# Kernel optimization log

Hardware: AMD Instinct MI355X
Metric: run time of the kernel (lower is better)

## Reference

```python
import math
import jax, jax.numpy as jnp
import numpy as np

B, N, D = 32, 1025, 768
K, CD, TD = 64, 128, 256  # num_clusters, cluster_dim, token_dim
REG = 0.1
NUM_ITERS = 5


def setup_inputs() -> dict:
    key = jax.random.key(0)
    ks = jax.random.split(key, 8)
    x = jax.random.normal(ks[0], (B, N, D), dtype=jnp.float32)
    # Linear params (torch nn.Linear: y = x @ W.T + b; we store W already transposed as [in, out])
    Wf = jax.random.normal(ks[1], (D, CD), dtype=jnp.float32) / math.sqrt(D)
    bf = jnp.zeros((CD,), dtype=jnp.float32)
    Ws = jax.random.normal(ks[2], (D, K), dtype=jnp.float32) / math.sqrt(D)
    bs = jnp.zeros((K,), dtype=jnp.float32)
    Wt = jax.random.normal(ks[3], (D, TD), dtype=jnp.float32) / math.sqrt(D)
    bt = jnp.zeros((TD,), dtype=jnp.float32)
    anchors = jax.random.normal(ks[4], (K, CD), dtype=jnp.float32) * 0.1
    dust_bin = jnp.float32(1.0)
    sharpness = jnp.float32(5.0)
    return {"x": x, "Wf": Wf, "bf": bf, "Ws": Ws, "bs": bs, "Wt": Wt, "bt": bt,
            "anchors": anchors, "dust_bin": dust_bin, "sharpness": sharpness}


def _log_otp_solver(log_a, log_b, M, num_iters, reg):
    M = M / reg
    u = jnp.zeros_like(log_a)  # [B, K+1]
    v = jnp.zeros_like(log_b)  # [B, N-1]
    for _ in range(num_iters):
        u = log_a - jax.nn.logsumexp(M + v[:, None, :], axis=2)
        v = log_b - jax.nn.logsumexp(M + u[:, :, None], axis=1)
    return M + u[:, :, None] + v[:, None, :]


def reference(x, Wf, bf, Ws, bs, Wt, bt, anchors, dust_bin, sharpness):
    b, n, d = x.shape
    t_global = x[:, 0]            # [B, D]
    fi = x[:, 1:]                 # [B, N-1, D]
    f = fi @ Wf + bf              # [B, N-1, CD]
    s = jnp.swapaxes(fi @ Ws + bs, 1, 2)  # [B, K, N-1]
    t = t_global @ Wt + bt        # [B, TD]
    s = s * sharpness
    dust = jnp.broadcast_to(dust_bin, (b, 1, n - 1))
    s_aug = jnp.concatenate([s, dust], axis=1)  # [B, K+1, N-1]
    log_a = jnp.full((b, K + 1), -math.log(K + 1), dtype=x.dtype)
    log_b = jnp.full((b, n - 1), -math.log(n - 1), dtype=x.dtype)
    log_P = _log_otp_solver(log_a, log_b, s_aug, NUM_ITERS, REG)
    p = jnp.exp(log_P)[:, :-1, :]  # [B, K, N-1]
    # v_agg = sum_n p[b,k,n] * (2*f[b,n,:] - anchors[k,:])  (algebraic rewrite of the broadcast sum)
    v_agg = 2.0 * jnp.einsum('bkn,bnc->bkc', p, f) - p.sum(axis=2)[:, :, None] * anchors[None]
    v_local = v_agg.reshape(b, -1)            # [B, K*CD]
    f_out = jnp.concatenate([t, v_local], axis=-1)
    norm = jnp.maximum(jnp.linalg.norm(f_out, axis=-1, keepdims=True), 1e-12)
    return f_out / norm
```

## Files before the change

kernel.cpp:

```cpp
#include <hip/hip_runtime.h>
#include <math.h>


#define BATCH 32
#define NTOK  1025
#define DIM   768
#define KDIM  64
#define CDIM  128
#define TDIM  256
#define NM1   1024
#define ROWLEN 8448
#define NITER 5
#define INV_REG 10.0f
#define NS_AGG 8
#define LOG_A (-4.17438727f)
#define LOG_B (-6.93147181f)

typedef __attribute__((ext_vector_type(8))) short short8;
typedef __attribute__((ext_vector_type(4))) float floatx4;

typedef __attribute__((address_space(3))) unsigned int lds_uint;
typedef const __attribute__((address_space(1))) unsigned int glb_uint;

__device__ __forceinline__ void gload_lds16(const void* g, void* l) {
    __builtin_amdgcn_global_load_lds((glb_uint*)g, (lds_uint*)l, 16, 0, 0);
}

__device__ __forceinline__ unsigned short bf16_rne(float f) {
    unsigned u = __builtin_bit_cast(unsigned, f);
    unsigned r = u + 0x7FFFu + ((u >> 16) & 1u);
    return (unsigned short)(r >> 16);
}

__device__ __forceinline__ short8 cvt8(float4 a, float4 b) {
    short8 r;
    r[0] = (short)bf16_rne(a.x); r[1] = (short)bf16_rne(a.y);
    r[2] = (short)bf16_rne(a.z); r[3] = (short)bf16_rne(a.w);
    r[4] = (short)bf16_rne(b.x); r[5] = (short)bf16_rne(b.y);
    r[6] = (short)bf16_rne(b.z); r[7] = (short)bf16_rne(b.w);
    return r;
}

__global__ __launch_bounds__(256) void prep(
    const float* __restrict__ Wf, const float* __restrict__ Ws,
    const float* __restrict__ bf, const float* __restrict__ bs,
    const float* __restrict__ x, const float* __restrict__ Wt,
    short* __restrict__ W_pack, float* __restrict__ bias_all,
    float* __restrict__ tpart)
{
    __shared__ float xr[256];
    const int blk = blockIdx.x, tid = threadIdx.x;
    if (blk < 576) {
        int idx = blk * 256 + tid;
        int g    = idx / 6144;
        int rem  = idx - g * 6144;
        int nf   = rem >> 9;
        int rem2 = rem & 511;
        int lane = rem2 >> 3;
        int j    = rem2 & 7;
        int k = g * 32 + (lane >> 4) * 8 + j;
        int c = nf * 16 + (lane & 15);
        float v = (c < CDIM) ? Wf[(size_t)k * CDIM + c] : Ws[(size_t)k * KDIM + (c - CDIM)];
        W_pack[idx] = (short)bf16_rne(v);
        if (idx < 192) bias_all[idx] = (idx < CDIM) ? bf[idx] : bs[idx - CDIM];
    } else {
        int i = blk - 576;
        int b = i / 3, dy = i - b * 3;
        xr[tid] = x[(size_t)b * NTOK * DIM + (size_t)dy * 256 + tid];
        __syncthreads();
        float acc = 0.f;
        const float* wp = Wt + (size_t)dy * 256 * TDIM + tid;
#pragma unroll 8
        for (int d = 0; d < 256; ++d) acc = fmaf(xr[d], wp[(size_t)d * TDIM], acc);
        tpart[((size_t)dy * BATCH + b) * TDIM + tid] = acc;
    }
}

__global__ __launch_bounds__(256, 2) void gemm_fs(
    const float* __restrict__ x, const short* __restrict__ W_pack,
    const float* __restrict__ bias_all, const float* __restrict__ sharp_p,
    unsigned short* __restrict__ fT, float* __restrict__ Mmat)
{
    __shared__ __align__(16) short Bs[12288];
    __shared__ __align__(16) short As[4096];
    const int tid  = threadIdx.x;
    const int wave = tid >> 6, lane = tid & 63;
    const int quad = lane >> 4, lrow = lane & 15;
    const int R = blockIdx.x * 64 + wave * 16;

    const int arow = blockIdx.x * 64 + (tid >> 2);
    const float* asrc = x + ((size_t)(arow >> 10) * NTOK + 1 + (arow & 1023)) * DIM + (tid & 3) * 16;
    const int r    = (tid >> 2) & 15;
    const int seg  = tid & 3;
    const int kk_w = seg >> 1;
    const int q0   = (seg & 1) * 2;
    short* adst0 = &As[(((tid >> 6) * 2 + kk_w) * 64 + q0 * 16 + r) * 8];
    short* adst1 = &As[(((tid >> 6) * 2 + kk_w) * 64 + (q0 + 1) * 16 + r) * 8];

    floatx4 acc[12];
#pragma unroll
    for (int nf = 0; nf < 12; ++nf) acc[nf] = (floatx4){0.f, 0.f, 0.f, 0.f};

    float4 g0 = *(const float4*)(asrc);
    float4 g1 = *(const float4*)(asrc + 4);
    float4 g2 = *(const float4*)(asrc + 8);
    float4 g3 = *(const float4*)(asrc + 12);

    for (int ko = 0; ko < 12; ++ko) {
        __syncthreads();
        const short* bsrc = W_pack + ko * 12288 + tid * 8;
#pragma unroll
        for (int i = 0; i < 6; ++i)
            gload_lds16(bsrc + i * 2048, &Bs[i * 2048 + tid * 8]);
        *(short8*)adst0 = cvt8(g0, g1);
        *(short8*)adst1 = cvt8(g2, g3);
        if (ko < 11) {
            const float* ap = asrc + (ko + 1) * 64;
            g0 = *(const float4*)(ap);
            g1 = *(const float4*)(ap + 4);
            g2 = *(const float4*)(ap + 8);
            g3 = *(const float4*)(ap + 12);
        }
        __syncthreads();
#pragma unroll
        for (int kk = 0; kk < 2; ++kk) {
            short8 af = *(const short8*)&As[((wave * 2 + kk) * 64 + lane) * 8];
#pragma unroll
            for (int nf = 0; nf < 12; ++nf) {
                short8 bf8 = *(const short8*)&Bs[((kk * 12 + nf) * 64 + lane) * 8];
                acc[nf] = __builtin_amdgcn_mfma_f32_16x16x32_bf16(af, bf8, acc[nf], 0, 0, 0);
            }
        }
    }

    const float sc = sharp_p[0] * INV_REG;
    const int bb = R >> 10;
    const int tok = (R & 1023) + quad * 4;
#pragma unroll
    for (int nf = 0; nf < 12; ++nf) {
        const int c = nf * 16 + lrow;
        const float bias = bias_all[c];
        if (nf < 8) {
            ushort4 w;
            w.x = bf16_rne(acc[nf][0] + bias);
            w.y = bf16_rne(acc[nf][1] + bias);
            w.z = bf16_rne(acc[nf][2] + bias);
            w.w = bf16_rne(acc[nf][3] + bias);
            *(ushort4*)(fT + ((size_t)bb * CDIM + c) * NM1 + tok) = w;
        } else {
            const int k = c - CDIM;
            float4 w = make_float4((acc[nf][0] + bias) * sc, (acc[nf][1] + bias) * sc,
                                   (acc[nf][2] + bias) * sc, (acc[nf][3] + bias) * sc);
            *(float4*)(Mmat + ((size_t)bb * KDIM + k) * NM1 + tok) = w;
        }
    }
}

template<bool FIRST>
__global__ __launch_bounds__(256) void sink_u(
    const float* __restrict__ Mmat, const float* __restrict__ v_in,
    const float* __restrict__ dust_p, float* __restrict__ u_out)
{
    const int wv   = (blockIdx.x << 2) + (threadIdx.x >> 6);
    const int lane = threadIdx.x & 63;
    const int b = wv / 65, k = wv - b * 65;
    const float dustM = dust_p[0] * INV_REG;

    const float4* vp = (const float4*)(v_in + (size_t)b * NM1);
    float xs[16];
    if (k < 64) {
        const float4* Mp = (const float4*)(Mmat + ((size_t)b * KDIM + k) * NM1);
#pragma unroll
        for (int i = 0; i < 4; ++i) {
            float4 mv = Mp[i * 64 + lane];
            float4 vv = FIRST ? make_float4(0.f, 0.f, 0.f, 0.f) : vp[i * 64 + lane];
            xs[i * 4 + 0] = mv.x + vv.x;
            xs[i * 4 + 1] = mv.y + vv.y;
            xs[i * 4 + 2] = mv.z + vv.z;
            xs[i * 4 + 3] = mv.w + vv.w;
        }
    } else {
#pragma unroll
        for (int i = 0; i < 4; ++i) {
            float4 vv = FIRST ? make_float4(0.f, 0.f, 0.f, 0.f) : vp[i * 64 + lane];
            xs[i * 4 + 0] = dustM + vv.x;
            xs[i * 4 + 1] = dustM + vv.y;
            xs[i * 4 + 2] = dustM + vv.z;
            xs[i * 4 + 3] = dustM + vv.w;
        }
    }
    float m = xs[0];
#pragma unroll
    for (int i = 1; i < 16; ++i) m = fmaxf(m, xs[i]);
#pragma unroll
    for (int off = 1; off < 64; off <<= 1) m = fmaxf(m, __shfl_xor(m, off));
    float S = 0.f;
#pragma unroll
    for (int i = 0; i < 16; ++i) S += __expf(xs[i] - m);
#pragma unroll
    for (int off = 1; off < 64; off <<= 1) S += __shfl_xor(S, off);
    if (lane == 0) u_out[wv] = LOG_A - (m + __logf(S));
}

__global__ __launch_bounds__(128) void sink_v(
    const float* __restrict__ Mmat, const float* __restrict__ u_in,
    const float* __restrict__ dust_p, float* __restrict__ v_out)
{
    __shared__ float us[65];
    const int b = blockIdx.x, tid = threadIdx.x;
    const int n = blockIdx.y * 128 + tid;
    if (tid < 65) us[tid] = u_in[b * 65 + tid];
    __syncthreads();
    const float* Mb = Mmat + (size_t)b * KDIM * NM1 + n;
    float xs[64];
#pragma unroll
    for (int k = 0; k < 64; ++k) xs[k] = Mb[(size_t)k * NM1] + us[k];
    const float xd = dust_p[0] * INV_REG + us[64];
    float m = xd;
#pragma unroll
    for (int k = 0; k < 64; ++k) m = fmaxf(m, xs[k]);
    float S = __expf(xd - m);
#pragma unroll
    for (int k = 0; k < 64; ++k) S += __expf(xs[k] - m);
    v_out[(size_t)b * NM1 + n] = LOG_B - (m + __logf(S));
}

__global__ __launch_bounds__(256) void aggregate(
    const float* __restrict__ Mmat, const unsigned short* __restrict__ fT,
    const float* __restrict__ u_in, const float* __restrict__ v_in,
    float* __restrict__ vpart, float* __restrict__ rspart)
{
    __shared__ float us[KDIM];
    __shared__ float vsh[128];
    const int b = blockIdx.x, ns = blockIdx.y;
    const int tid = threadIdx.x;
    const int wave = tid >> 6, lane = tid & 63;
    const int quad = lane >> 4, lrow = lane & 15;

    if (tid < 64) us[tid] = u_in[b * 65 + tid];
    else if (tid < 192) vsh[tid - 64] = v_in[(size_t)b * NM1 + ns * 128 + (tid - 64)];
    __syncthreads();

    const int krow = wave * 16 + lrow;
    const float uk = us[krow];
    const float* Mrow = Mmat + ((size_t)b * KDIM + krow) * NM1 + ns * 128 + quad * 8;
    const unsigned short* fbase = fT + ((size_t)b * CDIM + lrow) * NM1 + ns * 128 + quad * 8;

    floatx4 acc[8];
#pragma unroll
    for (int nf = 0; nf < 8; ++nf) acc[nf] = (floatx4){0.f, 0.f, 0.f, 0.f};
    float rs = 0.f;

#pragma unroll
    for (int step = 0; step < 4; ++step) {
        const float* mp = Mrow + step * 32;
        float4 m0 = *(const float4*)(mp);
        float4 m1 = *(const float4*)(mp + 4);
        const int tb = step * 32 + quad * 8;
        float p[8];
        p[0] = __expf(m0.x + uk + vsh[tb + 0]);
        p[1] = __expf(m0.y + uk + vsh[tb + 1]);
        p[2] = __expf(m0.z + uk + vsh[tb + 2]);
        p[3] = __expf(m0.w + uk + vsh[tb + 3]);
        p[4] = __expf(m1.x + uk + vsh[tb + 4]);
        p[5] = __expf(m1.y + uk + vsh[tb + 5]);
        p[6] = __expf(m1.z + uk + vsh[tb + 6]);
        p[7] = __expf(m1.w + uk + vsh[tb + 7]);
        short8 afrag;
#pragma unroll
        for (int j = 0; j < 8; ++j) {
            rs += p[j];
            afrag[j] = (short)bf16_rne(p[j]);
        }
#pragma unroll
        for (int nf = 0; nf < 8; ++nf) {
            short8 bfrag = *(const short8*)(fbase + (size_t)nf * 16 * NM1 + step * 32);
            acc[nf] = __builtin_amdgcn_mfma_f32_16x16x32_bf16(afrag, bfrag, acc[nf], 0, 0, 0);
        }
    }

    rs += __shfl_xor(rs, 16);
    rs += __shfl_xor(rs, 32);
    if (lane < 16) rspart[(ns * BATCH + b) * KDIM + krow] = rs;

    float* vp = vpart + (size_t)(ns * BATCH + b) * (KDIM * CDIM);
#pragma unroll
    for (int nf = 0; nf < 8; ++nf) {
        const int c = nf * 16 + lrow;
#pragma unroll
        for (int j = 0; j < 4; ++j)
            vp[(size_t)(wave * 16 + quad * 4 + j) * CDIM + c] = acc[nf][j];
    }
}

__global__ __launch_bounds__(1024) void finalize_all(
    const float* __restrict__ vpart, const float* __restrict__ rspart,
    const float* __restrict__ anchors, const float* __restrict__ tpart,
    const float* __restrict__ bt, float* __restrict__ out)
{
    __shared__ float rstot[KDIM];
    __shared__ float red[16];
    __shared__ float sc_sh;
    const int b = blockIdx.x, tid = threadIdx.x;
    const int lane = tid & 63, wave = tid >> 6;

    if (tid < KDIM) {
        float s = 0.f;
#pragma unroll
        for (int ns = 0; ns < NS_AGG; ++ns)
            s += rspart[(ns * BATCH + b) * KDIM + tid];
        rstot[tid] = s;
    }
    __syncthreads();

    const size_t e0 = (size_t)tid * 8;
    float4 s0 = make_float4(0.f, 0.f, 0.f, 0.f);
    float4 s1 = make_float4(0.f, 0.f, 0.f, 0.f);
#pragma unroll
    for (int ns = 0; ns < NS_AGG; ++ns) {
        const float* vp = vpart + (size_t)(ns * BATCH + b) * (KDIM * CDIM) + e0;
        float4 a = *(const float4*)(vp);
        float4 c = *(const float4*)(vp + 4);
        s0.x += a.x; s0.y += a.y; s0.z += a.z; s0.w += a.w;
        s1.x += c.x; s1.y += c.y; s1.z += c.z; s1.w += c.w;
    }
    const float rsv = rstot[tid >> 4];
    float4 a0 = *(const float4*)(anchors + e0);
    float4 a1 = *(const float4*)(anchors + e0 + 4);
    float4 v0, v1;
    v0.x = 2.f * s0.x - rsv * a0.x;  v0.y = 2.f * s0.y - rsv * a0.y;
    v0.z = 2.f * s0.z - rsv * a0.z;  v0.w = 2.f * s0.w - rsv * a0.w;
    v1.x = 2.f * s1.x - rsv * a1.x;  v1.y = 2.f * s1.y - rsv * a1.y;
    v1.z = 2.f * s1.z - rsv * a1.z;  v1.w = 2.f * s1.w - rsv * a1.w;
    float ss = v0.x*v0.x + v0.y*v0.y + v0.z*v0.z + v0.w*v0.w
             + v1.x*v1.x + v1.y*v1.y + v1.z*v1.z + v1.w*v1.w;

    float t = 0.f;
    if (tid < TDIM) {
        t = bt[tid];
#pragma unroll
        for (int s = 0; s < 3; ++s) t += tpart[((size_t)s * BATCH + b) * TDIM + tid];
        ss += t * t;
    }

#pragma unroll
    for (int off = 32; off > 0; off >>= 1) ss += __shfl_down(ss, off);
    if (lane == 0) red[wave] = ss;
    __syncthreads();
    if (tid == 0) {
        float tot = 0.f;
#pragma unroll
        for (int i = 0; i < 16; ++i) tot += red[i];
        sc_sh = 1.f / fmaxf(sqrtf(tot), 1e-12f);
    }
    __syncthreads();
    const float scale = sc_sh;

    float* orow = out + (size_t)b * ROWLEN;
    if (tid < TDIM) orow[tid] = t * scale;
    v0.x *= scale; v0.y *= scale; v0.z *= scale; v0.w *= scale;
    v1.x *= scale; v1.y *= scale; v1.z *= scale; v1.w *= scale;
    *(float4*)&orow[TDIM + e0]     = v0;
    *(float4*)&orow[TDIM + e0 + 4] = v1;
}

extern "C" void kernel_launch(void* const* d_in, const int* in_sizes, int n_in,
                              void* d_out, int out_size, void* d_ws, size_t ws_size,
                              hipStream_t stream)
{
    const float* x       = (const float*)d_in[0];
    const float* Wf      = (const float*)d_in[1];
    const float* bf      = (const float*)d_in[2];
    const float* Ws      = (const float*)d_in[3];
    const float* bs      = (const float*)d_in[4];
    const float* Wt      = (const float*)d_in[5];
    const float* bt      = (const float*)d_in[6];
    const float* anchors = (const float*)d_in[7];
    const float* dust    = (const float*)d_in[8];
    const float* sharp   = (const float*)d_in[9];
    float* out = (float*)d_out;

    char* base = (char*)d_ws;
    short* W_pack        = (short*)base;
    float* bias_all      = (float*)(base + 294912);
    float* Mmat          = bias_all + 192;
    unsigned short* fT   = (unsigned short*)(Mmat + (size_t)BATCH * KDIM * NM1);
    float* u_buf         = (float*)(fT + (size_t)BATCH * CDIM * NM1);
    float* v_buf         = u_buf + BATCH * 65;
    float* vpart         = v_buf + BATCH * NM1;
    float* rspart        = vpart + (size_t)NS_AGG * BATCH * KDIM * CDIM;
    float* tpart         = rspart + NS_AGG * BATCH * KDIM;

    hipLaunchKernelGGL(prep, dim3(672), dim3(256), 0, stream,
                       Wf, Ws, bf, bs, x, Wt, W_pack, bias_all, tpart);
    hipLaunchKernelGGL(gemm_fs, dim3(512), dim3(256), 0, stream,
                       x, W_pack, bias_all, sharp, fT, Mmat);

    hipLaunchKernelGGL(HIP_KERNEL_NAME(sink_u<true>), dim3(520), dim3(256), 0, stream,
                       Mmat, v_buf, dust, u_buf);
    hipLaunchKernelGGL(sink_v, dim3(BATCH, 8), dim3(128), 0, stream,
                       Mmat, u_buf, dust, v_buf);
    for (int it = 1; it < NITER; ++it) {
        hipLaunchKernelGGL(HIP_KERNEL_NAME(sink_u<false>), dim3(520), dim3(256), 0, stream,
                           Mmat, v_buf, dust, u_buf);
        hipLaunchKernelGGL(sink_v, dim3(BATCH, 8), dim3(128), 0, stream,
                           Mmat, u_buf, dust, v_buf);
    }

    hipLaunchKernelGGL(aggregate, dim3(BATCH, NS_AGG), dim3(256), 0, stream,
                       Mmat, fT, u_buf, v_buf, vpart, rspart);
    hipLaunchKernelGGL(finalize_all, dim3(BATCH), dim3(1024), 0, stream,
                       vpart, rspart, anchors, tpart, bt, out);
}
```

Measured before the change: 243.8 us.

## Fuse final Sinkhorn v-step into aggregate and batch-major block ordering

```diff
diff --git a/kernel.cpp b/kernel.cpp
--- a/kernel.cpp
+++ b/kernel.cpp
@@ -86,9 +86,11 @@
     const int tid  = threadIdx.x;
     const int wave = tid >> 6, lane = tid & 63;
     const int quad = lane >> 4, lrow = lane & 15;
-    const int R = blockIdx.x * 64 + wave * 16;
-
-    const int arow = blockIdx.x * 64 + (tid >> 2);
+    const int bb0   = blockIdx.x & 31;
+    const int chunk = blockIdx.x >> 5;
+    const int R = bb0 * 1024 + chunk * 64 + wave * 16;
+
+    const int arow = bb0 * 1024 + chunk * 64 + (tid >> 2);
     const float* asrc = x + ((size_t)(arow >> 10) * NTOK + 1 + (arow & 1023)) * DIM + (tid & 3) * 16;
     const int r    = (tid >> 2) & 15;
     const int seg  = tid & 3;
@@ -161,9 +163,11 @@
     const float* __restrict__ Mmat, const float* __restrict__ v_in,
     const float* __restrict__ dust_p, float* __restrict__ u_out)
 {
-    const int wv   = (blockIdx.x << 2) + (threadIdx.x >> 6);
+    const int b   = blockIdx.x & 31;
+    const int sub = blockIdx.x >> 5;
+    const int k   = sub * 4 + (threadIdx.x >> 6);
+    if (k > 64) return;
     const int lane = threadIdx.x & 63;
-    const int b = wv / 65, k = wv - b * 65;
     const float dustM = dust_p[0] * INV_REG;
 
     const float4* vp = (const float4*)(v_in + (size_t)b * NM1);
@@ -199,73 +203,130 @@
     for (int i = 0; i < 16; ++i) S += __expf(xs[i] - m);
 #pragma unroll
     for (int off = 1; off < 64; off <<= 1) S += __shfl_xor(S, off);
-    if (lane == 0) u_out[wv] = LOG_A - (m + __logf(S));
-}
-
-__global__ __launch_bounds__(128) void sink_v(
+    if (lane == 0) u_out[b * 65 + k] = LOG_A - (m + __logf(S));
+}
+
+__global__ __launch_bounds__(256) void sink_v(
     const float* __restrict__ Mmat, const float* __restrict__ u_in,
     const float* __restrict__ dust_p, float* __restrict__ v_out)
 {
     __shared__ float us[65];
-    const int b = blockIdx.x, tid = threadIdx.x;
-    const int n = blockIdx.y * 128 + tid;
+    __shared__ float2 pp[4][64];
+    const int b   = blockIdx.x & 31;
+    const int ns2 = blockIdx.x >> 5;
+    const int tid = threadIdx.x;
+    const int tok = tid & 63, kq = tid >> 6;
+    const int n = ns2 * 64 + tok;
     if (tid < 65) us[tid] = u_in[b * 65 + tid];
     __syncthreads();
-    const float* Mb = Mmat + (size_t)b * KDIM * NM1 + n;
-    float xs[64];
-#pragma unroll
-    for (int k = 0; k < 64; ++k) xs[k] = Mb[(size_t)k * NM1] + us[k];
-    const float xd = dust_p[0] * INV_REG + us[64];
-    float m = xd;
-#pragma unroll
-    for (int k = 0; k < 64; ++k) m = fmaxf(m, xs[k]);
-    float S = __expf(xd - m);
-#pragma unroll
-    for (int k = 0; k < 64; ++k) S += __expf(xs[k] - m);
-    v_out[(size_t)b * NM1 + n] = LOG_B - (m + __logf(S));
+    const float* Mb = Mmat + ((size_t)b * KDIM + kq * 16) * NM1 + n;
+    float xs[16];
+#pragma unroll
+    for (int kk = 0; kk < 16; ++kk) xs[kk] = Mb[(size_t)kk * NM1] + us[kq * 16 + kk];
+    float m = xs[0];
+#pragma unroll
+    for (int kk = 1; kk < 16; ++kk) m = fmaxf(m, xs[kk]);
+    float e = 0.f;
+#pragma unroll
+    for (int kk = 0; kk < 16; ++kk) e += __expf(xs[kk] - m);
+    pp[kq][tok] = make_float2(m, e);
+    __syncthreads();
+    if (tid < 64) {
+        const float xd = dust_p[0] * INV_REG + us[64];
+        float m3 = xd;
+#pragma unroll
+        for (int q = 0; q < 4; ++q) m3 = fmaxf(m3, pp[q][tid].x);
+        float S3 = __expf(xd - m3);
+#pragma unroll
+        for (int q = 0; q < 4; ++q) S3 += pp[q][tid].y * __expf(pp[q][tid].x - m3);
+        v_out[(size_t)b * NM1 + ns2 * 64 + tid] = LOG_B - (m3 + __logf(S3));
+    }
 }
 
 __global__ __launch_bounds__(256) void aggregate(
     const float* __restrict__ Mmat, const unsigned short* __restrict__ fT,
-    const float* __restrict__ u_in, const float* __restrict__ v_in,
+    const float* __restrict__ u_in, const float* __restrict__ dust_p,
     float* __restrict__ vpart, float* __restrict__ rspart)
 {
-    __shared__ float us[KDIM];
-    __shared__ float vsh[128];
+    __shared__ float us[65];
+    __shared__ __align__(16) float vsh[128];
+    __shared__ float wv[4][128][2];
     const int b = blockIdx.x, ns = blockIdx.y;
     const int tid = threadIdx.x;
     const int wave = tid >> 6, lane = tid & 63;
     const int quad = lane >> 4, lrow = lane & 15;
-
-    if (tid < 64) us[tid] = u_in[b * 65 + tid];
-    else if (tid < 192) vsh[tid - 64] = v_in[(size_t)b * NM1 + ns * 128 + (tid - 64)];
-    __syncthreads();
-
     const int krow = wave * 16 + lrow;
+    const float dustM = dust_p[0] * INV_REG;
+
+    if (tid < 65) us[tid] = u_in[b * 65 + tid];
+    __syncthreads();
+
+    float mreg[32];
+    {
+        const float* Mrow = Mmat + ((size_t)b * KDIM + krow) * NM1 + ns * 128 + quad * 8;
+#pragma unroll
+        for (int s = 0; s < 4; ++s) {
+            float4 a = *(const float4*)(Mrow + s * 32);
+            float4 c = *(const float4*)(Mrow + s * 32 + 4);
+            mreg[s*8+0]=a.x; mreg[s*8+1]=a.y; mreg[s*8+2]=a.z; mreg[s*8+3]=a.w;
+            mreg[s*8+4]=c.x; mreg[s*8+5]=c.y; mreg[s*8+6]=c.z; mreg[s*8+7]=c.w;
+        }
+    }
+
     const float uk = us[krow];
-    const float* Mrow = Mmat + ((size_t)b * KDIM + krow) * NM1 + ns * 128 + quad * 8;
+#pragma unroll
+    for (int s = 0; s < 4; ++s) {
+#pragma unroll
+        for (int j = 0; j < 8; ++j) {
+            float x = mreg[s*8+j] + uk;
+            float m2 = x;
+            m2 = fmaxf(m2, __shfl_xor(m2, 1));
+            m2 = fmaxf(m2, __shfl_xor(m2, 2));
+            m2 = fmaxf(m2, __shfl_xor(m2, 4));
+            m2 = fmaxf(m2, __shfl_xor(m2, 8));
+            float e = __expf(x - m2);
+            e += __shfl_xor(e, 1);
+            e += __shfl_xor(e, 2);
+            e += __shfl_xor(e, 4);
+            e += __shfl_xor(e, 8);
+            if (lrow == 0) {
+                wv[wave][s*32 + quad*8 + j][0] = m2;
+                wv[wave][s*32 + quad*8 + j][1] = e;
+            }
+        }
+    }
+    __syncthreads();
+    if (tid < 128) {
+        const float xd = dustM + us[64];
+        float m3 = xd;
+#pragma unroll
+        for (int w = 0; w < 4; ++w) m3 = fmaxf(m3, wv[w][tid][0]);
+        float S3 = __expf(xd - m3);
+#pragma unroll
+        for (int w = 0; w < 4; ++w) S3 += wv[w][tid][1] * __expf(wv[w][tid][0] - m3);
+        vsh[tid] = LOG_B - (m3 + __logf(S3));
+    }
+    __syncthreads();
+
     const unsigned short* fbase = fT + ((size_t)b * CDIM + lrow) * NM1 + ns * 128 + quad * 8;
-
     floatx4 acc[8];
 #pragma unroll
     for (int nf = 0; nf < 8; ++nf) acc[nf] = (floatx4){0.f, 0.f, 0.f, 0.f};
     float rs = 0.f;
-
-#pragma unroll
-    for (int step = 0; step < 4; ++step) {
-        const float* mp = Mrow + step * 32;
-        float4 m0 = *(const float4*)(mp);
-        float4 m1 = *(const float4*)(mp + 4);
-        const int tb = step * 32 + quad * 8;
+#pragma unroll
+    for (int s = 0; s < 4; ++s) {
+        const int tb = s * 32 + quad * 8;
+        float4 v0 = *(const float4*)&vsh[tb];
+        float4 v1 = *(const float4*)&vsh[tb + 4];
         float p[8];
-        p[0] = __expf(m0.x + uk + vsh[tb + 0]);
-        p[1] = __expf(m0.y + uk + vsh[tb + 1]);
-        p[2] = __expf(m0.z + uk + vsh[tb + 2]);
-        p[3] = __expf(m0.w + uk + vsh[tb + 3]);
-        p[4] = __expf(m1.x + uk + vsh[tb + 4]);
-        p[5] = __expf(m1.y + uk + vsh[tb + 5]);
-        p[6] = __expf(m1.z + uk + vsh[tb + 6]);
-        p[7] = __expf(m1.w + uk + vsh[tb + 7]);
+        p[0] = __expf(mreg[s*8+0] + uk + v0.x);
+        p[1] = __expf(mreg[s*8+1] + uk + v0.y);
+        p[2] = __expf(mreg[s*8+2] + uk + v0.z);
+        p[3] = __expf(mreg[s*8+3] + uk + v0.w);
+        p[4] = __expf(mreg[s*8+4] + uk + v1.x);
+        p[5] = __expf(mreg[s*8+5] + uk + v1.y);
+        p[6] = __expf(mreg[s*8+6] + uk + v1.z);
+        p[7] = __expf(mreg[s*8+7] + uk + v1.w);
         short8 afrag;
 #pragma unroll
         for (int j = 0; j < 8; ++j) {
@@ -274,11 +335,10 @@
         }
 #pragma unroll
         for (int nf = 0; nf < 8; ++nf) {
-            short8 bfrag = *(const short8*)(fbase + (size_t)nf * 16 * NM1 + step * 32);
+            short8 bfrag = *(const short8*)(fbase + (size_t)nf * 16 * NM1 + s * 32);
             acc[nf] = __builtin_amdgcn_mfma_f32_16x16x32_bf16(afrag, bfrag, acc[nf], 0, 0, 0);
         }
     }
-
     rs += __shfl_xor(rs, 16);
     rs += __shfl_xor(rs, 32);
     if (lane < 16) rspart[(ns * BATCH + b) * KDIM + krow] = rs;
@@ -396,19 +456,17 @@
     hipLaunchKernelGGL(gemm_fs, dim3(512), dim3(256), 0, stream,
                        x, W_pack, bias_all, sharp, fT, Mmat);
 
-    hipLaunchKernelGGL(HIP_KERNEL_NAME(sink_u<true>), dim3(520), dim3(256), 0, stream,
+    hipLaunchKernelGGL(HIP_KERNEL_NAME(sink_u<true>), dim3(544), dim3(256), 0, stream,
                        Mmat, v_buf, dust, u_buf);
-    hipLaunchKernelGGL(sink_v, dim3(BATCH, 8), dim3(128), 0, stream,
-                       Mmat, u_buf, dust, v_buf);
     for (int it = 1; it < NITER; ++it) {
-        hipLaunchKernelGGL(HIP_KERNEL_NAME(sink_u<false>), dim3(520), dim3(256), 0, stream,
+        hipLaunchKernelGGL(sink_v, dim3(512), dim3(256), 0, stream,
+                           Mmat, u_buf, dust, v_buf);
+        hipLaunchKernelGGL(HIP_KERNEL_NAME(sink_u<false>), dim3(544), dim3(256), 0, stream,
                            Mmat, v_buf, dust, u_buf);
-        hipLaunchKernelGGL(sink_v, dim3(BATCH, 8), dim3(128), 0, stream,
-                           Mmat, u_buf, dust, v_buf);
     }
 
     hipLaunchKernelGGL(aggregate, dim3(BATCH, NS_AGG), dim3(256), 0, stream,
-                       Mmat, fT, u_buf, v_buf, vpart, rspart);
+                       Mmat, fT, u_buf, dust, vpart, rspart);
     hipLaunchKernelGGL(finalize_all, dim3(BATCH), dim3(1024), 0, stream,
                        vpart, rspart, anchors, tpart, bt, out);
 }
```

Measured after the change: 245.5 us. No clear change (+0.7%).
